# Optimization experiments

Hardware: AMD Instinct MI355X
Metric: run time of the kernel (lower is better)

## Reference

```python
import jax, jax.numpy as jnp
import numpy as np

DIM = 64
KSIZE = 3
BN_EPS = 1e-5

def _bn(x):
    # eval-mode BatchNorm2d with default running stats (mean=0, var=1) and affine (1, 0)
    return x / jnp.sqrt(1.0 + BN_EPS)

def _downsample(x, params):
    # four stride-2 3x3 convs: 3 -> 8 -> 16 -> 32 -> 64, BN after each, GELU except after last
    for i, (w, b) in enumerate(params):
        x = jax.lax.conv_general_dilated(x, w, (2, 2), ((1, 1), (1, 1))) + b[None, :, None, None]
        x = _bn(x)
        if i < 3:
            x = jax.nn.gelu(x, approximate=False)
    return x

def _attn(dx, q, kw, kb, vw, vb, pw, pb, dw, db):
    # single-head cross attention: learned queries q (1,T,C) attend to dx (B,N,C)
    scale = DIM ** -0.5
    k = dx @ kw.T + kb
    v = dx @ vw.T + vb
    a = jax.nn.softmax((q @ jnp.swapaxes(k, -1, -2)) * scale, axis=-1)  # (B,T,N)
    o = (a @ v) @ pw.T + pb                                            # (B,T,C)
    return o @ dw.T + db                                               # (B,T,1)

def _gk1d(sigma):
    half = (KSIZE - 1) * 0.5
    x = jnp.linspace(-half, half, KSIZE)
    pdf = jnp.exp(-0.5 * (x / sigma) ** 2)
    return pdf / pdf.sum()

def _gain_denoise(I1, r1, r2, gain, sigma):
    # per-image gain + gaussian-blur unsharp masking, vectorized over the batch
    def one(img, r1i, r2i, gi, si):
        ig = gi * img                                       # (3,H,W)
        k2 = _gk1d(r2i)[:, None] * _gk1d(r1i)[None, :]      # (k,k), sigma_x=r1, sigma_y=r2
        kern = jnp.broadcast_to(k2, (3, 1, KSIZE, KSIZE))   # depthwise kernel
        p = KSIZE // 2
        xp = jnp.pad(ig[None], ((0, 0), (0, 0), (p, p), (p, p)), mode='reflect')
        blur = jax.lax.conv_general_dilated(xp, kern, (1, 1), 'VALID', feature_group_count=3)[0]
        return blur + si * (img - blur)
    return jax.vmap(one)(I1, r1, r2, gain, sigma)

def setup_inputs():
    key = jax.random.key(0)
    ks = iter(jax.random.split(key, 64))
    def rn(shape, s=0.05):
        return jax.random.normal(next(ks), shape, dtype=jnp.float32) * s
    def ru(shape):
        return jax.random.uniform(next(ks), shape, dtype=jnp.float32)
    inp = {"I1": ru((8, 3, 512, 512))}
    for pre, T in (("kp", 4), ("mp", 10)):
        inp[pre + "_q"] = ru((1, T, DIM))
        chans = [3, DIM // 8, DIM // 4, DIM // 2, DIM]
        for i in range(4):
            inp[pre + "_c%dw" % (i + 1)] = rn((chans[i + 1], chans[i], 3, 3), 0.1)
            inp[pre + "_c%db" % (i + 1)] = jnp.zeros((chans[i + 1],), jnp.float32)
        for nm, shp in (("kw", (DIM, DIM)), ("vw", (DIM, DIM)), ("pw", (DIM, DIM)), ("dw", (1, DIM))):
            inp[pre + "_" + nm] = rn(shp)
        for nm, n in (("kb", DIM), ("vb", DIM), ("pb", DIM), ("db", 1)):
            inp[pre + "_" + nm] = jnp.zeros((n,), jnp.float32)
    inp["kp_gain_base"] = jnp.ones((1,), jnp.float32)  # mode='normal'
    dims = [3, 32, 32, 32, 32, 3]
    for i in range(5):
        inp["lut_w%d" % i] = rn((dims[i + 1], dims[i]), 0.2)
        inp["lut_b%d" % i] = jnp.zeros((dims[i + 1],), jnp.float32)
    return inp

def reference(I1, kp_q, kp_c1w, kp_c1b, kp_c2w, kp_c2b, kp_c3w, kp_c3b, kp_c4w, kp_c4b,
              kp_kw, kp_kb, kp_vw, kp_vb, kp_pw, kp_pb, kp_dw, kp_db, kp_gain_base,
              mp_q, mp_c1w, mp_c1b, mp_c2w, mp_c2b, mp_c3w, mp_c3b, mp_c4w, mp_c4b,
              mp_kw, mp_kb, mp_vw, mp_vb, mp_pw, mp_pb, mp_dw, mp_db,
              lut_w0, lut_b0, lut_w1, lut_b1, lut_w2, lut_b2, lut_w3, lut_b3, lut_w4, lut_b4):
    B = I1.shape[0]
    # --- Kernel_Predictor ---
    dx = _downsample(I1, [(kp_c1w, kp_c1b), (kp_c2w, kp_c2b), (kp_c3w, kp_c3b), (kp_c4w, kp_c4b)])
    dx = dx.reshape(B, DIM, -1).transpose(0, 2, 1)            # (B,N,C), N=(H/16)*(W/16)
    o = _attn(dx, kp_q, kp_kw, kp_kb, kp_vw, kp_vb, kp_pw, kp_pb, kp_dw, kp_db)[..., 0]  # (B,4)
    r1 = 0.1 * o[:, 0] + 3.0
    r2 = 0.1 * o[:, 1] + 2.0
    gain = o[:, 2] + kp_gain_base[0]
    sigma = jax.nn.sigmoid(o[:, 3])
    # --- gain + gaussian unsharp denoise ---
    I2 = jnp.clip(_gain_denoise(I1, r1, r2, gain, sigma), 1e-5, 1.0)
    # --- Matrix_Predictor ---
    dx2 = _downsample(I2, [(mp_c1w, mp_c1b), (mp_c2w, mp_c2b), (mp_c3w, mp_c3b), (mp_c4w, mp_c4b)])
    dx2 = dx2.reshape(B, DIM, -1).transpose(0, 2, 1)
    o2 = _attn(dx2, mp_q, mp_kw, mp_kb, mp_vw, mp_vb, mp_pw, mp_pb, mp_dw, mp_db)  # (B,10,1)
    ccm = 0.1 * o2[:, :9, 0].reshape(B, 3, 3) + jnp.eye(3, dtype=I1.dtype)
    dist = jax.nn.relu(o2[:, 9, 0]) + 1.0                     # (B,)
    # --- Shades-of-Gray white balance + CCM ---
    hwc = I2.transpose(0, 2, 3, 1)                            # (B,H,W,3)
    imgP = hwc ** dist[:, None, None, None]
    ch = jnp.mean(imgP, axis=(1, 2)) ** (1.0 / dist)[:, None]  # (B,3)
    avg = jnp.mean(imgP, axis=(1, 2, 3)) ** (1.0 / dist)       # (B,)
    I3 = hwc / (ch / avg[:, None])[:, None, None, :]
    I4 = jnp.clip(jnp.einsum('bhwc,bdc->bhwd', I3, ccm), 1e-5, 1.0)
    # --- NILUT residual per-pixel MLP ---
    h = jax.nn.relu(I4 @ lut_w0.T + lut_b0)
    h = jnp.tanh(h @ lut_w1.T + lut_b1)
    h = jnp.tanh(h @ lut_w2.T + lut_b2)
    h = jnp.tanh(h @ lut_w3.T + lut_b3)
    I5 = jnp.clip(h @ lut_w4.T + lut_b4 + I4, 0.0, 1.0)
    return I5.transpose(0, 3, 1, 2)                           # (B,3,H,W)
```

## Files before the change

kernel.cpp:

```cpp
#include <hip/hip_runtime.h>
#include <math.h>


#define BN_MUL 0.9999950000374997f

static constexpr int BB   = 8;
static constexpr int HH   = 512;
static constexpr int WW   = 512;
static constexpr int HW   = HH * WW;
static constexpr int NTOK = 1024;
static constexpr int DIMC = 64;

typedef _Float16 f16x8 __attribute__((ext_vector_type(8)));
typedef _Float16 f16x2 __attribute__((ext_vector_type(2)));
typedef float    f32x4 __attribute__((ext_vector_type(4)));

__device__ __forceinline__ float gelu_exact(float x) {
    return 0.5f * x * (1.0f + erff(x * 0.7071067811865476f));
}

__device__ __forceinline__ float tanh_fast(float x) {
    float e = __expf(2.0f * x);
    return 1.0f - 2.0f * __builtin_amdgcn_rcpf(e + 1.0f);
}

template<int Cin, int Hin, bool GELU>
__global__ __launch_bounds__(256) void conv_s2(const float* __restrict__ in,
                                               const float* __restrict__ wt,
                                               const float* __restrict__ bs,
                                               float* __restrict__ out)
{
    constexpr int Win  = Hin, Hout = Hin / 2, Wout = Hin / 2;
    constexpr int WSH  = (Wout == 256) ? 8 : (Wout == 128) ? 7 : (Wout == 64) ? 6 : 5;
    constexpr int PLANE = Hout * Wout;

    const int sp  = blockIdx.x * 256 + threadIdx.x;
    const int ow  = sp & (Wout - 1);
    const int oh  = sp >> WSH;
    const int oc0 = blockIdx.y * 4;
    const int b   = blockIdx.z;
    const int Cout = (int)gridDim.y * 4;

    float acc[4];
    #pragma unroll
    for (int o = 0; o < 4; ++o) acc[o] = bs[oc0 + o];

    const int ih0 = oh * 2 - 1, iw0 = ow * 2 - 1;
    const float fh0 = (ih0 >= 0) ? 1.f : 0.f;
    const float fw0 = (iw0 >= 0) ? 1.f : 0.f;
    const int r0 = (ih0 >= 0) ? ih0 : 0;
    const int cc0 = (iw0 >= 0) ? iw0 : 0;

    const float* ip = in + (size_t)(b * Cin) * Hin * Win;
    #pragma unroll
    for (int ic = 0; ic < Cin; ++ic) {
        const float* pl = ip + ic * Hin * Win;
        const float* p0 = pl + r0 * Win;
        const float* p1 = pl + (ih0 + 1) * Win;
        const float* p2 = pl + (ih0 + 2) * Win;
        float  v00 = p0[cc0] * (fh0 * fw0);
        float2 va  = *(const float2*)(p0 + iw0 + 1);
        float  v01 = va.x * fh0, v02 = va.y * fh0;
        float  v10 = p1[cc0] * fw0;
        float2 vb  = *(const float2*)(p1 + iw0 + 1);
        float  v20 = p2[cc0] * fw0;
        float2 vc  = *(const float2*)(p2 + iw0 + 1);
        #pragma unroll
        for (int o = 0; o < 4; ++o) {
            const float* wr = wt + ((oc0 + o) * Cin + ic) * 9;
            acc[o] += v00 * wr[0] + v01 * wr[1] + v02 * wr[2]
                    + v10 * wr[3] + vb.x * wr[4] + vb.y * wr[5]
                    + v20 * wr[6] + vc.x * wr[7] + vc.y * wr[8];
        }
    }
    #pragma unroll
    for (int o = 0; o < 4; ++o) {
        float a = acc[o] * BN_MUL;
        if (GELU) a = gelu_exact(a);
        out[(b * Cout + oc0 + o) * PLANE + sp] = a;
    }
}

__global__ __launch_bounds__(256) void attn_kv_kernel(const float* __restrict__ dx,
                               const float* __restrict__ kw, const float* __restrict__ kb,
                               const float* __restrict__ vw, const float* __restrict__ vb,
                               float* __restrict__ kout, float* __restrict__ vout)
{
    const int n = blockIdx.x * 256 + threadIdx.x;
    const int c = blockIdx.y;
    const int b = blockIdx.z;
    const float* dp  = dx + (b * DIMC) * NTOK + n;
    const float* kwr = kw + c * DIMC;
    const float* vwr = vw + c * DIMC;
    float ka = kb[c], va = vb[c];
    #pragma unroll
    for (int cc = 0; cc < DIMC; ++cc) {
        float d = dp[cc * NTOK];
        ka += d * kwr[cc];
        va += d * vwr[cc];
    }
    const int o = (b * DIMC + c) * NTOK + n;
    kout[o] = ka;
    vout[o] = va;
}

__global__ __launch_bounds__(1024) void attn_head_kernel(
                                 const float* __restrict__ kbuf, const float* __restrict__ vbuf,
                                 const float* __restrict__ q,
                                 const float* __restrict__ pw, const float* __restrict__ pb,
                                 const float* __restrict__ dw, const float* __restrict__ db,
                                 float* __restrict__ outv, int T)
{
    __shared__ float sc[NTOK];
    __shared__ float red[1024];
    __shared__ float qsh[DIMC];
    __shared__ float osh[DIMC];
    __shared__ float psh[DIMC];
    const int tid = threadIdx.x;
    const int bt  = blockIdx.x;
    const int b = bt / T, t = bt - b * T;

    if (tid < DIMC) qsh[tid] = q[t * DIMC + tid];
    __syncthreads();

    const float* kp = kbuf + (b * DIMC) * NTOK;
    const float* vp = vbuf + (b * DIMC) * NTOK;

    float s = 0.f;
    #pragma unroll
    for (int c = 0; c < DIMC; ++c) s += qsh[c] * kp[c * NTOK + tid];
    s *= 0.125f;

    red[tid] = s;
    __syncthreads();
    for (int off = 512; off > 0; off >>= 1) {
        if (tid < off) red[tid] = fmaxf(red[tid], red[tid + off]);
        __syncthreads();
    }
    float m = red[0];
    __syncthreads();

    float e = __expf(s - m);
    sc[tid] = e;
    red[tid] = e;
    __syncthreads();
    for (int off = 512; off > 0; off >>= 1) {
        if (tid < off) red[tid] += red[tid + off];
        __syncthreads();
    }
    float Ssum = red[0];
    __syncthreads();

    const int c  = tid & 63, qq = tid >> 6;
    float part = 0.f;
    const float* vr = vp + c * NTOK + qq * 64;
    const float* sr = sc + qq * 64;
    #pragma unroll
    for (int n = 0; n < 64; ++n) part += sr[n] * vr[n];
    red[tid] = part;
    __syncthreads();
    if (tid < DIMC) {
        float o = 0.f;
        #pragma unroll
        for (int k = 0; k < 16; ++k) o += red[tid + k * 64];
        osh[tid] = o / Ssum;
    }
    __syncthreads();
    if (tid < DIMC) {
        float p = pb[tid];
        const float* pwr = pw + tid * DIMC;
        #pragma unroll
        for (int cc = 0; cc < DIMC; ++cc) p += osh[cc] * pwr[cc];
        psh[tid] = p;
    }
    __syncthreads();
    if (tid == 0) {
        float r = db[0];
        #pragma unroll
        for (int cc = 0; cc < DIMC; ++cc) r += psh[cc] * dw[cc];
        outv[bt] = r;
    }
}

__global__ void denoise_kernel(const float* __restrict__ I1, const float* __restrict__ attno,
                               const float* __restrict__ gain_base, float* __restrict__ I2)
{
    const int idx = blockIdx.x * 256 + threadIdx.x;
    const int w  = idx & (WW - 1);
    const int h2 = (idx >> 9) & (HH / 2 - 1);
    const int t  = idx >> 17;
    const int b  = t / 3;

    const float o0 = attno[b * 4 + 0], o1 = attno[b * 4 + 1];
    const float o2 = attno[b * 4 + 2], o3 = attno[b * 4 + 3];
    const float r1 = 0.1f * o0 + 3.0f;
    const float r2 = 0.1f * o1 + 2.0f;
    const float g  = o2 + gain_base[0];
    const float sg = 1.0f / (1.0f + __expf(-o3));
    const float ex = __expf(-0.5f / (r1 * r1));
    const float nx = 1.0f / (2.0f * ex + 1.0f);
    const float ey = __expf(-0.5f / (r2 * r2));
    const float ny = 1.0f / (2.0f * ey + 1.0f);
    const float kx0 = ex * nx, kx1 = nx;
    const float ky0 = ey * ny, ky1 = ny;

    const int h0 = h2 * 2;
    const float* ip = I1 + (size_t)t * HW;
    int ra = h0 - 1; ra = (ra < 0) ? 1 : ra;
    int rd = h0 + 2; rd = (rd >= HH) ? (2 * HH - 2 - rd) : rd;
    int c0 = w - 1;  c0 = (c0 < 0) ? 1 : c0;
    int c2 = w + 1;  c2 = (c2 >= WW) ? (WW - 2) : c2;
    const int rows[4] = { ra, h0, h0 + 1, rd };

    float rs[4], vm[4];
    #pragma unroll
    for (int i = 0; i < 4; ++i) {
        const float* rp = ip + rows[i] * WW;
        float a = rp[c0], mday = rp[w], z = rp[c2];
        vm[i] = mday;
        rs[i] = kx0 * (a + z) + kx1 * mday;
    }
    float blur0 = g * (ky0 * (rs[0] + rs[2]) + ky1 * rs[1]);
    float blur1 = g * (ky0 * (rs[1] + rs[3]) + ky1 * rs[2]);
    float out0 = blur0 + sg * (vm[1] - blur0);
    float out1 = blur1 + sg * (vm[2] - blur1);
    out0 = fminf(fmaxf(out0, 1e-5f), 1.0f);
    out1 = fminf(fmaxf(out1, 1e-5f), 1.0f);
    float* op = I2 + (size_t)t * HW + h0 * WW + w;
    op[0]  = out0;
    op[WW] = out1;
}

__global__ void wb_reduce_kernel(const float* __restrict__ I2, const float* __restrict__ attno,
                                 float* __restrict__ sums)
{
    __shared__ float red[256];
    int b = blockIdx.y;
    float d = attno[b * 10 + 9];
    d = (d > 0.f ? d : 0.f) + 1.0f;
    float l0 = 0.f, l1 = 0.f, l2 = 0.f;
    const float* base = I2 + b * 3 * HW;
    for (int pix = blockIdx.x * blockDim.x + threadIdx.x; pix < HW; pix += blockDim.x * gridDim.x) {
        l0 += __expf(d * __logf(base[pix]));
        l1 += __expf(d * __logf(base[HW + pix]));
        l2 += __expf(d * __logf(base[2 * HW + pix]));
    }
    float loc[3] = {l0, l1, l2};
    for (int c = 0; c < 3; ++c) {
        red[threadIdx.x] = loc[c];
        __syncthreads();
        for (int off = 128; off > 0; off >>= 1) {
            if (threadIdx.x < off) red[threadIdx.x] += red[threadIdx.x + off];
            __syncthreads();
        }
        if (threadIdx.x == 0) atomicAdd(&sums[b * 4 + c], red[0]);
        __syncthreads();
    }
}

__global__ void wb_finalize_kernel(const float* __restrict__ sums, const float* __restrict__ attno,
                                   float* __restrict__ wbsc)
{
    int b = threadIdx.x;
    if (b >= BB) return;
    float d = attno[b * 10 + 9];
    d = (d > 0.f ? d : 0.f) + 1.0f;
    float inv = 1.0f / d;
    float s0 = sums[b * 4 + 0], s1 = sums[b * 4 + 1], s2 = sums[b * 4 + 2];
    float ch0 = powf(s0 / (float)HW, inv);
    float ch1 = powf(s1 / (float)HW, inv);
    float ch2 = powf(s2 / (float)HW, inv);
    float avg = powf((s0 + s1 + s2) / (3.0f * (float)HW), inv);
    wbsc[b * 4 + 0] = avg / ch0;
    wbsc[b * 4 + 1] = avg / ch1;
    wbsc[b * 4 + 2] = avg / ch2;
}

__global__ void __launch_bounds__(256) final_kernel(
    float* __restrict__ io,
    const float* __restrict__ wbsc, const float* __restrict__ attno,
    const float* __restrict__ w0, const float* __restrict__ b0,
    const float* __restrict__ w1, const float* __restrict__ b1,
    const float* __restrict__ w2, const float* __restrict__ b2,
    const float* __restrict__ w3, const float* __restrict__ b3,
    const float* __restrict__ w4, const float* __restrict__ b4)
{
    constexpr int ROW = 72;
    __shared__ __align__(16) _Float16 LDS[4][64 * ROW];
    const int tid  = threadIdx.x;
    const int wv   = tid >> 6;
    const int lane = tid & 63;
    const int nn   = lane & 15;
    const int quad = lane >> 4;
    _Float16* Wl = LDS[wv];

    const int b   = blockIdx.x >> 10;
    const int pix = (blockIdx.x * 256 + tid) & (HW - 1);
    float* base = io + b * 3 * HW + pix;

    const float s0 = wbsc[b * 4 + 0], s1 = wbsc[b * 4 + 1], s2 = wbsc[b * 4 + 2];
    float v0 = base[0] * s0;
    float v1 = base[HW] * s1;
    float v2 = base[2 * HW] * s2;
    const float* o2p = attno + b * 10;
    float I4[3];
    #pragma unroll
    for (int d = 0; d < 3; ++d) {
        float m0 = 0.1f * o2p[d * 3]     + (d == 0 ? 1.f : 0.f);
        float m1 = 0.1f * o2p[d * 3 + 1] + (d == 1 ? 1.f : 0.f);
        float m2 = 0.1f * o2p[d * 3 + 2] + (d == 2 ? 1.f : 0.f);
        I4[d] = fminf(fmaxf(m0 * v0 + m1 * v1 + m2 * v2, 1e-5f), 1.0f);
    }

    #pragma unroll
    for (int j = 0; j < 32; j += 2) {
        float a0 = b0[j]   + w0[j*3]     * I4[0] + w0[j*3+1]     * I4[1] + w0[j*3+2]     * I4[2];
        float a1 = b0[j+1] + w0[(j+1)*3] * I4[0] + w0[(j+1)*3+1] * I4[1] + w0[(j+1)*3+2] * I4[2];
        f16x2 p;
        p[0] = (_Float16)fmaxf(a0, 0.f);
        p[1] = (_Float16)fmaxf(a1, 0.f);
        *(f16x2*)&Wl[lane * ROW + j] = p;
    }

    f16x8 wf[3][2];
    float bv[3][2];
    const float* wls[3] = { w1, w2, w3 };
    const float* bls[3] = { b1, b2, b3 };
    #pragma unroll
    for (int L = 0; L < 3; ++L) {
        #pragma unroll
        for (int h = 0; h < 2; ++h) {
            const float* wr = wls[L] + (16 * h + nn) * 32 + quad * 8;
            #pragma unroll
            for (int i = 0; i < 8; ++i) wf[L][h][i] = (_Float16)wr[i];
            bv[L][h] = bls[L][16 * h + nn];
        }
    }
    __syncthreads();

    #pragma unroll
    for (int L = 0; L < 3; ++L) {
        f16x8 af[4];
        #pragma unroll
        for (int t = 0; t < 4; ++t)
            af[t] = *(const f16x8*)&Wl[(16 * t + nn) * ROW + quad * 8];
        __syncthreads();
        #pragma unroll
        for (int t = 0; t < 4; ++t) {
            #pragma unroll
            for (int h = 0; h < 2; ++h) {
                f32x4 c;
                c[0] = c[1] = c[2] = c[3] = bv[L][h];
                f32x4 d = __builtin_amdgcn_mfma_f32_16x16x32_f16(af[t], wf[L][h], c, 0, 0, 0);
                #pragma unroll
                for (int r = 0; r < 4; ++r)
                    Wl[(16 * t + quad * 4 + r) * ROW + 16 * h + nn] = (_Float16)tanh_fast(d[r]);
            }
        }
        __syncthreads();
    }

    float h4[32];
    #pragma unroll
    for (int g = 0; g < 4; ++g) {
        f16x8 rv = *(const f16x8*)&Wl[lane * ROW + g * 8];
        #pragma unroll
        for (int i = 0; i < 8; ++i) h4[g * 8 + i] = (float)rv[i];
    }
    #pragma unroll
    for (int d = 0; d < 3; ++d) {
        float a = b4[d];
        const float* wr = w4 + d * 32;
        #pragma unroll
        for (int k = 0; k < 32; ++k) a += h4[k] * wr[k];
        a += I4[d];
        base[d * HW] = fminf(fmaxf(a, 0.f), 1.0f);
    }
}

extern "C" void kernel_launch(void* const* d_in, const int* in_sizes, int n_in,
                              void* d_out, int out_size, void* d_ws, size_t ws_size,
                              hipStream_t stream)
{
    const float* I1      = (const float*)d_in[0];
    const float* kp_q    = (const float*)d_in[1];
    const float* kp_c1w  = (const float*)d_in[2];  const float* kp_c1b = (const float*)d_in[3];
    const float* kp_c2w  = (const float*)d_in[4];  const float* kp_c2b = (const float*)d_in[5];
    const float* kp_c3w  = (const float*)d_in[6];  const float* kp_c3b = (const float*)d_in[7];
    const float* kp_c4w  = (const float*)d_in[8];  const float* kp_c4b = (const float*)d_in[9];
    const float* kp_kw   = (const float*)d_in[10]; const float* kp_vw  = (const float*)d_in[11];
    const float* kp_pw   = (const float*)d_in[12]; const float* kp_dw  = (const float*)d_in[13];
    const float* kp_kb   = (const float*)d_in[14]; const float* kp_vb  = (const float*)d_in[15];
    const float* kp_pb   = (const float*)d_in[16]; const float* kp_db  = (const float*)d_in[17];
    const float* mp_q    = (const float*)d_in[18];
    const float* mp_c1w  = (const float*)d_in[19]; const float* mp_c1b = (const float*)d_in[20];
    const float* mp_c2w  = (const float*)d_in[21]; const float* mp_c2b = (const float*)d_in[22];
    const float* mp_c3w  = (const float*)d_in[23]; const float* mp_c3b = (const float*)d_in[24];
    const float* mp_c4w  = (const float*)d_in[25]; const float* mp_c4b = (const float*)d_in[26];
    const float* mp_kw   = (const float*)d_in[27]; const float* mp_vw  = (const float*)d_in[28];
    const float* mp_pw   = (const float*)d_in[29]; const float* mp_dw  = (const float*)d_in[30];
    const float* mp_kb   = (const float*)d_in[31]; const float* mp_vb  = (const float*)d_in[32];
    const float* mp_pb   = (const float*)d_in[33]; const float* mp_db  = (const float*)d_in[34];
    const float* gainb   = (const float*)d_in[35];
    const float* lw0 = (const float*)d_in[36]; const float* lb0 = (const float*)d_in[37];
    const float* lw1 = (const float*)d_in[38]; const float* lb1 = (const float*)d_in[39];
    const float* lw2 = (const float*)d_in[40]; const float* lb2 = (const float*)d_in[41];
    const float* lw3 = (const float*)d_in[42]; const float* lb3 = (const float*)d_in[43];
    const float* lw4 = (const float*)d_in[44]; const float* lb4 = (const float*)d_in[45];

    float* ws    = (float*)d_ws;
    float* ds1   = ws;
    float* ds2   = ds1 + 8 * 8 * 256 * 256;
    float* ds3   = ds2 + 8 * 16 * 128 * 128;
    float* ds4   = ds3 + 8 * 32 * 64 * 64;
    float* kbuf  = ds4 + 8 * 64 * 32 * 32;
    float* vbuf  = kbuf + 8 * 64 * 1024;
    float* attno = vbuf + 8 * 64 * 1024;
    float* sums  = attno + 128;
    float* wbsc  = sums + 32;
    float* I2    = (float*)d_out;

    conv_s2<3, 512, true ><<<dim3(256, 2, BB), 256, 0, stream>>>(I1,  kp_c1w, kp_c1b, ds1);
    conv_s2<8, 256, true ><<<dim3(64,  4, BB), 256, 0, stream>>>(ds1, kp_c2w, kp_c2b, ds2);
    conv_s2<16, 128, true><<<dim3(16,  8, BB), 256, 0, stream>>>(ds2, kp_c3w, kp_c3b, ds3);
    conv_s2<32, 64, false><<<dim3(4,  16, BB), 256, 0, stream>>>(ds3, kp_c4w, kp_c4b, ds4);
    attn_kv_kernel<<<dim3(NTOK / 256, DIMC, BB), 256, 0, stream>>>(ds4, kp_kw, kp_kb, kp_vw, kp_vb, kbuf, vbuf);
    attn_head_kernel<<<BB * 4, 1024, 0, stream>>>(kbuf, vbuf, kp_q, kp_pw, kp_pb, kp_dw, kp_db, attno, 4);

    denoise_kernel<<<(BB * 3 * HW / 2) / 256, 256, 0, stream>>>(I1, attno, gainb, I2);

    conv_s2<3, 512, true ><<<dim3(256, 2, BB), 256, 0, stream>>>(I2,  mp_c1w, mp_c1b, ds1);
    conv_s2<8, 256, true ><<<dim3(64,  4, BB), 256, 0, stream>>>(ds1, mp_c2w, mp_c2b, ds2);
    conv_s2<16, 128, true><<<dim3(16,  8, BB), 256, 0, stream>>>(ds2, mp_c3w, mp_c3b, ds3);
    conv_s2<32, 64, false><<<dim3(4,  16, BB), 256, 0, stream>>>(ds3, mp_c4w, mp_c4b, ds4);
    attn_kv_kernel<<<dim3(NTOK / 256, DIMC, BB), 256, 0, stream>>>(ds4, mp_kw, mp_kb, mp_vw, mp_vb, kbuf, vbuf);
    attn_head_kernel<<<BB * 10, 1024, 0, stream>>>(kbuf, vbuf, mp_q, mp_pw, mp_pb, mp_dw, mp_db, attno, 10);

    (void)hipMemsetAsync(sums, 0, 32 * sizeof(float), stream);
    wb_reduce_kernel<<<dim3(64, BB), 256, 0, stream>>>(I2, attno, sums);
    wb_finalize_kernel<<<1, 64, 0, stream>>>(sums, attno, wbsc);

    final_kernel<<<BB * HW / 256, 256, 0, stream>>>(I2, wbsc, attno,
        lw0, lb0, lw1, lb1, lw2, lb2, lw3, lb3, lw4, lb4);
}
```

Baseline: 459.0 us.

## Fuse denoise with first conv, fold K/V projections into attention, drop WB kernels

Merges the denoise pass with the first stride-2 conv of the second branch, so I2 is written once and conv1 reads its blurred values from registers instead of reloading them. The K/V projection kernel is replaced algebraically: q is folded through kw (and kb), and the value projection is applied after the softmax-weighted sum, so the K/V buffers are never built. The white-balance reduction now writes per-chunk partial sums without atomics or a memset, and the finalize step moves into the final kernel. Early conv layers compute 8 output channels per thread. The costs are redundant stencil reads in the fused kernel, every final_kernel thread re-summing the partials, and slightly different float rounding from the reordered maths.

```diff
diff --git a/kernel.cpp b/kernel.cpp
--- a/kernel.cpp
+++ b/kernel.cpp
@@ -10,6 +10,7 @@
 static constexpr int HW   = HH * WW;
 static constexpr int NTOK = 1024;
 static constexpr int DIMC = 64;
+static constexpr int WBCH = 32;
 
 typedef _Float16 f16x8 __attribute__((ext_vector_type(8)));
 typedef _Float16 f16x2 __attribute__((ext_vector_type(2)));
@@ -24,7 +25,7 @@
     return 1.0f - 2.0f * __builtin_amdgcn_rcpf(e + 1.0f);
 }
 
-template<int Cin, int Hin, bool GELU>
+template<int Cin, int Hin, int OCT, bool GELU>
 __global__ __launch_bounds__(256) void conv_s2(const float* __restrict__ in,
                                                const float* __restrict__ wt,
                                                const float* __restrict__ bs,
@@ -37,13 +38,13 @@
     const int sp  = blockIdx.x * 256 + threadIdx.x;
     const int ow  = sp & (Wout - 1);
     const int oh  = sp >> WSH;
-    const int oc0 = blockIdx.y * 4;
+    const int oc0 = blockIdx.y * OCT;
     const int b   = blockIdx.z;
-    const int Cout = (int)gridDim.y * 4;
-
-    float acc[4];
-    #pragma unroll
-    for (int o = 0; o < 4; ++o) acc[o] = bs[oc0 + o];
+    const int Cout = (int)gridDim.y * OCT;
+
+    float acc[OCT];
+    #pragma unroll
+    for (int o = 0; o < OCT; ++o) acc[o] = bs[oc0 + o];
 
     const int ih0 = oh * 2 - 1, iw0 = ow * 2 - 1;
     const float fh0 = (ih0 >= 0) ? 1.f : 0.f;
@@ -66,7 +67,7 @@
         float  v20 = p2[cc0] * fw0;
         float2 vc  = *(const float2*)(p2 + iw0 + 1);
         #pragma unroll
-        for (int o = 0; o < 4; ++o) {
+        for (int o = 0; o < OCT; ++o) {
             const float* wr = wt + ((oc0 + o) * Cin + ic) * 9;
             acc[o] += v00 * wr[0] + v01 * wr[1] + v02 * wr[2]
                     + v10 * wr[3] + vb.x * wr[4] + vb.y * wr[5]
@@ -74,122 +75,23 @@
         }
     }
     #pragma unroll
-    for (int o = 0; o < 4; ++o) {
+    for (int o = 0; o < OCT; ++o) {
         float a = acc[o] * BN_MUL;
         if (GELU) a = gelu_exact(a);
         out[(b * Cout + oc0 + o) * PLANE + sp] = a;
     }
 }
 
-__global__ __launch_bounds__(256) void attn_kv_kernel(const float* __restrict__ dx,
-                               const float* __restrict__ kw, const float* __restrict__ kb,
-                               const float* __restrict__ vw, const float* __restrict__ vb,
-                               float* __restrict__ kout, float* __restrict__ vout)
-{
-    const int n = blockIdx.x * 256 + threadIdx.x;
-    const int c = blockIdx.y;
-    const int b = blockIdx.z;
-    const float* dp  = dx + (b * DIMC) * NTOK + n;
-    const float* kwr = kw + c * DIMC;
-    const float* vwr = vw + c * DIMC;
-    float ka = kb[c], va = vb[c];
-    #pragma unroll
-    for (int cc = 0; cc < DIMC; ++cc) {
-        float d = dp[cc * NTOK];
-        ka += d * kwr[cc];
-        va += d * vwr[cc];
-    }
-    const int o = (b * DIMC + c) * NTOK + n;
-    kout[o] = ka;
-    vout[o] = va;
-}
-
-__global__ __launch_bounds__(1024) void attn_head_kernel(
-                                 const float* __restrict__ kbuf, const float* __restrict__ vbuf,
-                                 const float* __restrict__ q,
-                                 const float* __restrict__ pw, const float* __restrict__ pb,
-                                 const float* __restrict__ dw, const float* __restrict__ db,
-                                 float* __restrict__ outv, int T)
-{
-    __shared__ float sc[NTOK];
-    __shared__ float red[1024];
-    __shared__ float qsh[DIMC];
-    __shared__ float osh[DIMC];
-    __shared__ float psh[DIMC];
-    const int tid = threadIdx.x;
-    const int bt  = blockIdx.x;
-    const int b = bt / T, t = bt - b * T;
-
-    if (tid < DIMC) qsh[tid] = q[t * DIMC + tid];
-    __syncthreads();
-
-    const float* kp = kbuf + (b * DIMC) * NTOK;
-    const float* vp = vbuf + (b * DIMC) * NTOK;
-
-    float s = 0.f;
-    #pragma unroll
-    for (int c = 0; c < DIMC; ++c) s += qsh[c] * kp[c * NTOK + tid];
-    s *= 0.125f;
-
-    red[tid] = s;
-    __syncthreads();
-    for (int off = 512; off > 0; off >>= 1) {
-        if (tid < off) red[tid] = fmaxf(red[tid], red[tid + off]);
-        __syncthreads();
-    }
-    float m = red[0];
-    __syncthreads();
-
-    float e = __expf(s - m);
-    sc[tid] = e;
-    red[tid] = e;
-    __syncthreads();
-    for (int off = 512; off > 0; off >>= 1) {
-        if (tid < off) red[tid] += red[tid + off];
-        __syncthreads();
-    }
-    float Ssum = red[0];
-    __syncthreads();
-
-    const int c  = tid & 63, qq = tid >> 6;
-    float part = 0.f;
-    const float* vr = vp + c * NTOK + qq * 64;
-    const float* sr = sc + qq * 64;
-    #pragma unroll
-    for (int n = 0; n < 64; ++n) part += sr[n] * vr[n];
-    red[tid] = part;
-    __syncthreads();
-    if (tid < DIMC) {
-        float o = 0.f;
-        #pragma unroll
-        for (int k = 0; k < 16; ++k) o += red[tid + k * 64];
-        osh[tid] = o / Ssum;
-    }
-    __syncthreads();
-    if (tid < DIMC) {
-        float p = pb[tid];
-        const float* pwr = pw + tid * DIMC;
-        #pragma unroll
-        for (int cc = 0; cc < DIMC; ++cc) p += osh[cc] * pwr[cc];
-        psh[tid] = p;
-    }
-    __syncthreads();
-    if (tid == 0) {
-        float r = db[0];
-        #pragma unroll
-        for (int cc = 0; cc < DIMC; ++cc) r += psh[cc] * dw[cc];
-        outv[bt] = r;
-    }
-}
-
-__global__ void denoise_kernel(const float* __restrict__ I1, const float* __restrict__ attno,
-                               const float* __restrict__ gain_base, float* __restrict__ I2)
-{
-    const int idx = blockIdx.x * 256 + threadIdx.x;
-    const int w  = idx & (WW - 1);
-    const int h2 = (idx >> 9) & (HH / 2 - 1);
-    const int t  = idx >> 17;
-    const int b  = t / 3;
+__global__ __launch_bounds__(256) void denoise_conv1_kernel(
+    const float* __restrict__ I1, const float* __restrict__ attno,
+    const float* __restrict__ gain_base,
+    const float* __restrict__ wt, const float* __restrict__ bs,
+    float* __restrict__ I2, float* __restrict__ out)
+{
+    const int sp = blockIdx.x * 256 + threadIdx.x;
+    const int ow = sp & 255;
+    const int oh = sp >> 8;
+    const int b  = blockIdx.z;
 
     const float o0 = attno[b * 4 + 0], o1 = attno[b * 4 + 1];
     const float o2 = attno[b * 4 + 2], o3 = attno[b * 4 + 3];
@@ -204,81 +106,193 @@
     const float kx0 = ex * nx, kx1 = nx;
     const float ky0 = ey * ny, ky1 = ny;
 
-    const int h0 = h2 * 2;
-    const float* ip = I1 + (size_t)t * HW;
-    int ra = h0 - 1; ra = (ra < 0) ? 1 : ra;
-    int rd = h0 + 2; rd = (rd >= HH) ? (2 * HH - 2 - rd) : rd;
-    int c0 = w - 1;  c0 = (c0 < 0) ? 1 : c0;
-    int c2 = w + 1;  c2 = (c2 >= WW) ? (WW - 2) : c2;
-    const int rows[4] = { ra, h0, h0 + 1, rd };
-
-    float rs[4], vm[4];
-    #pragma unroll
-    for (int i = 0; i < 4; ++i) {
-        const float* rp = ip + rows[i] * WW;
-        float a = rp[c0], mday = rp[w], z = rp[c2];
-        vm[i] = mday;
-        rs[i] = kx0 * (a + z) + kx1 * mday;
-    }
-    float blur0 = g * (ky0 * (rs[0] + rs[2]) + ky1 * rs[1]);
-    float blur1 = g * (ky0 * (rs[1] + rs[3]) + ky1 * rs[2]);
-    float out0 = blur0 + sg * (vm[1] - blur0);
-    float out1 = blur1 + sg * (vm[2] - blur1);
-    out0 = fminf(fmaxf(out0, 1e-5f), 1.0f);
-    out1 = fminf(fmaxf(out1, 1e-5f), 1.0f);
-    float* op = I2 + (size_t)t * HW + h0 * WW + w;
-    op[0]  = out0;
-    op[WW] = out1;
-}
-
-__global__ void wb_reduce_kernel(const float* __restrict__ I2, const float* __restrict__ attno,
-                                 float* __restrict__ sums)
+    const int rbase = 2 * oh - 2, cbase = 2 * ow - 2;
+    int ri[5], ci[5];
+    #pragma unroll
+    for (int i = 0; i < 5; ++i) {
+        int r = rbase + i; ri[i] = r < 0 ? -r : (r > 511 ? 1022 - r : r);
+        int c = cbase + i; ci[i] = c < 0 ? -c : (c > 511 ? 1022 - c : c);
+    }
+    const bool topE = (oh == 0), leftE = (ow == 0);
+
+    float acc[8];
+    #pragma unroll
+    for (int o = 0; o < 8; ++o) acc[o] = bs[o];
+
+    #pragma unroll
+    for (int c = 0; c < 3; ++c) {
+        const float* ip = I1 + ((size_t)b * 3 + c) * HW;
+        float p[5][5];
+        #pragma unroll
+        for (int i = 0; i < 5; ++i) {
+            const float* rp = ip + ri[i] * WW;
+            #pragma unroll
+            for (int j = 0; j < 5; ++j) p[i][j] = rp[ci[j]];
+        }
+        float hs[5][3];
+        #pragma unroll
+        for (int i = 0; i < 5; ++i)
+            #pragma unroll
+            for (int j = 0; j < 3; ++j)
+                hs[i][j] = kx0 * (p[i][j] + p[i][j + 2]) + kx1 * p[i][j + 1];
+        float w2[3][3];
+        #pragma unroll
+        for (int i = 0; i < 3; ++i)
+            #pragma unroll
+            for (int j = 0; j < 3; ++j) {
+                float bl = g * (ky0 * (hs[i][j] + hs[i + 2][j]) + ky1 * hs[i + 1][j]);
+                float val = bl + sg * (p[i + 1][j + 1] - bl);
+                w2[i][j] = fminf(fmaxf(val, 1e-5f), 1.0f);
+            }
+        float* op = I2 + ((size_t)b * 3 + c) * HW + (2 * oh) * WW + 2 * ow;
+        float2 w0v; w0v.x = w2[1][1]; w0v.y = w2[1][2];
+        float2 w1v; w1v.x = w2[2][1]; w1v.y = w2[2][2];
+        *(float2*)op        = w0v;
+        *(float2*)(op + WW) = w1v;
+        if (topE)  { w2[0][0] = 0.f; w2[0][1] = 0.f; w2[0][2] = 0.f; }
+        if (leftE) { w2[0][0] = 0.f; w2[1][0] = 0.f; w2[2][0] = 0.f; }
+        #pragma unroll
+        for (int o = 0; o < 8; ++o) {
+            const float* wr = wt + (o * 3 + c) * 9;
+            acc[o] += w2[0][0] * wr[0] + w2[0][1] * wr[1] + w2[0][2] * wr[2]
+                    + w2[1][0] * wr[3] + w2[1][1] * wr[4] + w2[1][2] * wr[5]
+                    + w2[2][0] * wr[6] + w2[2][1] * wr[7] + w2[2][2] * wr[8];
+        }
+    }
+    #pragma unroll
+    for (int o = 0; o < 8; ++o)
+        out[(b * 8 + o) * 65536 + sp] = gelu_exact(acc[o] * BN_MUL);
+}
+
+__global__ __launch_bounds__(1024) void attn_kernel(
+    const float* __restrict__ dx, const float* __restrict__ q,
+    const float* __restrict__ kw, const float* __restrict__ kb,
+    const float* __restrict__ vw, const float* __restrict__ vb,
+    const float* __restrict__ pw, const float* __restrict__ pb,
+    const float* __restrict__ dw, const float* __restrict__ db,
+    float* __restrict__ outv, int T)
+{
+    __shared__ float qk[DIMC];
+    __shared__ float red[1024];
+    __shared__ float sc[NTOK];
+    __shared__ float uN[DIMC];
+    __shared__ float osh[DIMC];
+    __shared__ float psh[DIMC];
+    __shared__ float qkb_s;
+    const int tid = threadIdx.x;
+    const int bt  = blockIdx.x;
+    const int b = bt / T, t = bt - b * T;
+    const float* qt = q + t * DIMC;
+
+    if (tid < DIMC) {
+        float s = 0.f;
+        #pragma unroll
+        for (int c = 0; c < DIMC; ++c) s += qt[c] * kw[c * DIMC + tid];
+        qk[tid] = s;
+    }
+    if (tid == 1023) {
+        float s = 0.f;
+        #pragma unroll
+        for (int c = 0; c < DIMC; ++c) s += qt[c] * kb[c];
+        qkb_s = s;
+    }
+    __syncthreads();
+
+    const float* dp = dx + (size_t)(b * DIMC) * NTOK;
+    float s = qkb_s;
+    #pragma unroll
+    for (int c = 0; c < DIMC; ++c) s += qk[c] * dp[c * NTOK + tid];
+    s *= 0.125f;
+
+    red[tid] = s;
+    __syncthreads();
+    for (int off = 512; off > 0; off >>= 1) {
+        if (tid < off) red[tid] = fmaxf(red[tid], red[tid + off]);
+        __syncthreads();
+    }
+    float m = red[0];
+    __syncthreads();
+
+    float e = __expf(s - m);
+    sc[tid] = e;
+    red[tid] = e;
+    __syncthreads();
+    for (int off = 512; off > 0; off >>= 1) {
+        if (tid < off) red[tid] += red[tid + off];
+        __syncthreads();
+    }
+    float Ssum = red[0];
+    __syncthreads();
+
+    const int c  = tid & 63, qq = tid >> 6;
+    float part = 0.f;
+    const float* dr = dp + c * NTOK + qq * 64;
+    const float* sr = sc + qq * 64;
+    #pragma unroll
+    for (int n = 0; n < 64; ++n) part += sr[n] * dr[n];
+    red[tid] = part;
+    __syncthreads();
+    if (tid < DIMC) {
+        float u = 0.f;
+        #pragma unroll
+        for (int k = 0; k < 16; ++k) u += red[tid + k * 64];
+        uN[tid] = u / Ssum;
+    }
+    __syncthreads();
+    if (tid < DIMC) {
+        float o = vb[tid];
+        const float* vr = vw + tid * DIMC;
+        #pragma unroll
+        for (int cc = 0; cc < DIMC; ++cc) o += vr[cc] * uN[cc];
+        osh[tid] = o;
+    }
+    __syncthreads();
+    if (tid < DIMC) {
+        float p = pb[tid];
+        const float* pr = pw + tid * DIMC;
+        #pragma unroll
+        for (int cc = 0; cc < DIMC; ++cc) p += pr[cc] * osh[cc];
+        psh[tid] = p;
+    }
+    __syncthreads();
+    if (tid == 0) {
+        float r = db[0];
+        #pragma unroll
+        for (int cc = 0; cc < DIMC; ++cc) r += psh[cc] * dw[cc];
+        outv[bt] = r;
+    }
+}
+
+__global__ __launch_bounds__(256) void wb_reduce_kernel(const float* __restrict__ I2,
+                                                        const float* __restrict__ attno,
+                                                        float* __restrict__ part)
 {
     __shared__ float red[256];
-    int b = blockIdx.y;
+    const int bc = blockIdx.y;
+    const int b  = bc / 3;
     float d = attno[b * 10 + 9];
-    d = (d > 0.f ? d : 0.f) + 1.0f;
-    float l0 = 0.f, l1 = 0.f, l2 = 0.f;
-    const float* base = I2 + b * 3 * HW;
-    for (int pix = blockIdx.x * blockDim.x + threadIdx.x; pix < HW; pix += blockDim.x * gridDim.x) {
-        l0 += __expf(d * __logf(base[pix]));
-        l1 += __expf(d * __logf(base[HW + pix]));
-        l2 += __expf(d * __logf(base[2 * HW + pix]));
-    }
-    float loc[3] = {l0, l1, l2};
-    for (int c = 0; c < 3; ++c) {
-        red[threadIdx.x] = loc[c];
+    d = fmaxf(d, 0.f) + 1.0f;
+    constexpr int CHUNK = HW / WBCH;
+    const float4* base = (const float4*)(I2 + (size_t)bc * HW + blockIdx.x * CHUNK);
+    float l = 0.f;
+    #pragma unroll
+    for (int i = threadIdx.x, it = 0; it < CHUNK / 4 / 256; ++it, i += 256) {
+        float4 v = base[i];
+        l += __expf(d * __logf(v.x)) + __expf(d * __logf(v.y))
+           + __expf(d * __logf(v.z)) + __expf(d * __logf(v.w));
+    }
+    red[threadIdx.x] = l;
+    __syncthreads();
+    for (int off = 128; off > 0; off >>= 1) {
+        if (threadIdx.x < off) red[threadIdx.x] += red[threadIdx.x + off];
         __syncthreads();
-        for (int off = 128; off > 0; off >>= 1) {
-            if (threadIdx.x < off) red[threadIdx.x] += red[threadIdx.x + off];
-            __syncthreads();
-        }
-        if (threadIdx.x == 0) atomicAdd(&sums[b * 4 + c], red[0]);
-        __syncthreads();
-    }
-}
-
-__global__ void wb_finalize_kernel(const float* __restrict__ sums, const float* __restrict__ attno,
-                                   float* __restrict__ wbsc)
-{
-    int b = threadIdx.x;
-    if (b >= BB) return;
-    float d = attno[b * 10 + 9];
-    d = (d > 0.f ? d : 0.f) + 1.0f;
-    float inv = 1.0f / d;
-    float s0 = sums[b * 4 + 0], s1 = sums[b * 4 + 1], s2 = sums[b * 4 + 2];
-    float ch0 = powf(s0 / (float)HW, inv);
-    float ch1 = powf(s1 / (float)HW, inv);
-    float ch2 = powf(s2 / (float)HW, inv);
-    float avg = powf((s0 + s1 + s2) / (3.0f * (float)HW), inv);
-    wbsc[b * 4 + 0] = avg / ch0;
-    wbsc[b * 4 + 1] = avg / ch1;
-    wbsc[b * 4 + 2] = avg / ch2;
+    }
+    if (threadIdx.x == 0) part[bc * WBCH + blockIdx.x] = red[0];
 }
 
 __global__ void __launch_bounds__(256) final_kernel(
     float* __restrict__ io,
-    const float* __restrict__ wbsc, const float* __restrict__ attno,
+    const float* __restrict__ part, const float* __restrict__ attno,
     const float* __restrict__ w0, const float* __restrict__ b0,
     const float* __restrict__ w1, const float* __restrict__ b1,
     const float* __restrict__ w2, const float* __restrict__ b2,
@@ -298,11 +312,26 @@
     const int pix = (blockIdx.x * 256 + tid) & (HW - 1);
     float* base = io + b * 3 * HW + pix;
 
-    const float s0 = wbsc[b * 4 + 0], s1 = wbsc[b * 4 + 1], s2 = wbsc[b * 4 + 2];
-    float v0 = base[0] * s0;
-    float v1 = base[HW] * s1;
-    float v2 = base[2 * HW] * s2;
     const float* o2p = attno + b * 10;
+    float dd = fmaxf(o2p[9], 0.f) + 1.0f;
+    float inv = 1.0f / dd;
+    float s[3];
+    #pragma unroll
+    for (int c = 0; c < 3; ++c) {
+        float t0 = 0.f;
+        const float* pp = part + (b * 3 + c) * WBCH;
+        #pragma unroll
+        for (int k = 0; k < WBCH; ++k) t0 += pp[k];
+        s[c] = t0;
+    }
+    const float avg = __expf(inv * __logf((s[0] + s[1] + s[2]) * (1.0f / (3.0f * HW))));
+    const float wb0 = avg / __expf(inv * __logf(s[0] * (1.0f / HW)));
+    const float wb1 = avg / __expf(inv * __logf(s[1] * (1.0f / HW)));
+    const float wb2 = avg / __expf(inv * __logf(s[2] * (1.0f / HW)));
+
+    float v0 = base[0] * wb0;
+    float v1 = base[HW] * wb1;
+    float v2 = base[2 * HW] * wb2;
     float I4[3];
     #pragma unroll
     for (int d = 0; d < 3; ++d) {
@@ -413,33 +442,28 @@
     float* ds2   = ds1 + 8 * 8 * 256 * 256;
     float* ds3   = ds2 + 8 * 16 * 128 * 128;
     float* ds4   = ds3 + 8 * 32 * 64 * 64;
-    float* kbuf  = ds4 + 8 * 64 * 32 * 32;
-    float* vbuf  = kbuf + 8 * 64 * 1024;
-    float* attno = vbuf + 8 * 64 * 1024;
-    float* sums  = attno + 128;
-    float* wbsc  = sums + 32;
+    float* attno = ds4 + 8 * 64 * 32 * 32;
+    float* part  = attno + 128;
     float* I2    = (float*)d_out;
 
-    conv_s2<3, 512, true ><<<dim3(256, 2, BB), 256, 0, stream>>>(I1,  kp_c1w, kp_c1b, ds1);
-    conv_s2<8, 256, true ><<<dim3(64,  4, BB), 256, 0, stream>>>(ds1, kp_c2w, kp_c2b, ds2);
-    conv_s2<16, 128, true><<<dim3(16,  8, BB), 256, 0, stream>>>(ds2, kp_c3w, kp_c3b, ds3);
-    conv_s2<32, 64, false><<<dim3(4,  16, BB), 256, 0, stream>>>(ds3, kp_c4w, kp_c4b, ds4);
-    attn_kv_kernel<<<dim3(NTOK / 256, DIMC, BB), 256, 0, stream>>>(ds4, kp_kw, kp_kb, kp_vw, kp_vb, kbuf, vbuf);
-    attn_head_kernel<<<BB * 4, 1024, 0, stream>>>(kbuf, vbuf, kp_q, kp_pw, kp_pb, kp_dw, kp_db, attno, 4);
-
-    denoise_kernel<<<(BB * 3 * HW / 2) / 256, 256, 0, stream>>>(I1, attno, gainb, I2);
-
-    conv_s2<3, 512, true ><<<dim3(256, 2, BB), 256, 0, stream>>>(I2,  mp_c1w, mp_c1b, ds1);
-    conv_s2<8, 256, true ><<<dim3(64,  4, BB), 256, 0, stream>>>(ds1, mp_c2w, mp_c2b, ds2);
-    conv_s2<16, 128, true><<<dim3(16,  8, BB), 256, 0, stream>>>(ds2, mp_c3w, mp_c3b, ds3);
-    conv_s2<32, 64, false><<<dim3(4,  16, BB), 256, 0, stream>>>(ds3, mp_c4w, mp_c4b, ds4);
-    attn_kv_kernel<<<dim3(NTOK / 256, DIMC, BB), 256, 0, stream>>>(ds4, mp_kw, mp_kb, mp_vw, mp_vb, kbuf, vbuf);
-    attn_head_kernel<<<BB * 10, 1024, 0, stream>>>(kbuf, vbuf, mp_q, mp_pw, mp_pb, mp_dw, mp_db, attno, 10);
-
-    (void)hipMemsetAsync(sums, 0, 32 * sizeof(float), stream);
-    wb_reduce_kernel<<<dim3(64, BB), 256, 0, stream>>>(I2, attno, sums);
-    wb_finalize_kernel<<<1, 64, 0, stream>>>(sums, attno, wbsc);
-
-    final_kernel<<<BB * HW / 256, 256, 0, stream>>>(I2, wbsc, attno,
+    conv_s2<3, 512, 8, true ><<<dim3(256, 1, BB), 256, 0, stream>>>(I1,  kp_c1w, kp_c1b, ds1);
+    conv_s2<8, 256, 8, true ><<<dim3(64,  2, BB), 256, 0, stream>>>(ds1, kp_c2w, kp_c2b, ds2);
+    conv_s2<16, 128, 4, true><<<dim3(16,  8, BB), 256, 0, stream>>>(ds2, kp_c3w, kp_c3b, ds3);
+    conv_s2<32, 64, 4, false><<<dim3(4,  16, BB), 256, 0, stream>>>(ds3, kp_c4w, kp_c4b, ds4);
+    attn_kernel<<<BB * 4, 1024, 0, stream>>>(ds4, kp_q, kp_kw, kp_kb, kp_vw, kp_vb,
+                                             kp_pw, kp_pb, kp_dw, kp_db, attno, 4);
+
+    denoise_conv1_kernel<<<dim3(256, 1, BB), 256, 0, stream>>>(I1, attno, gainb,
+                                                               mp_c1w, mp_c1b, I2, ds1);
+
+    conv_s2<8, 256, 8, true ><<<dim3(64,  2, BB), 256, 0, stream>>>(ds1, mp_c2w, mp_c2b, ds2);
+    conv_s2<16, 128, 4, true><<<dim3(16,  8, BB), 256, 0, stream>>>(ds2, mp_c3w, mp_c3b, ds3);
+    conv_s2<32, 64, 4, false><<<dim3(4,  16, BB), 256, 0, stream>>>(ds3, mp_c4w, mp_c4b, ds4);
+    attn_kernel<<<BB * 10, 1024, 0, stream>>>(ds4, mp_q, mp_kw, mp_kb, mp_vw, mp_vb,
+                                              mp_pw, mp_pb, mp_dw, mp_db, attno, 10);
+
+    wb_reduce_kernel<<<dim3(WBCH, 24), 256, 0, stream>>>(I2, attno, part);
+
+    final_kernel<<<BB * HW / 256, 256, 0, stream>>>(I2, part, attno,
         lw0, lb0, lw1, lb1, lw2, lb2, lw3, lb3, lw4, lb4);
 }
```

New measurement: 438.9 us. -4.4%, faster.
